# Optimization experiments

Hardware: AMD Instinct MI355X
Metric: run time of the kernel (lower is better)

## Reference

```python
import jax, jax.numpy as jnp
import numpy as np

EMBED = 768
HEADS = 12
HEAD_DIM = EMBED // HEADS
HIDDEN = int(EMBED * 4.0)
B, N = 2, 2048


def setup_inputs() -> dict:
    key = jax.random.key(0)
    ks = jax.random.split(key, 8)
    s = 0.02
    return {
        "x": jax.random.normal(ks[0], (B, N, EMBED), dtype=jnp.float32),
        "ln1_g": jnp.ones((EMBED,), jnp.float32),
        "ln1_b": jnp.zeros((EMBED,), jnp.float32),
        "qkv_w": jax.random.normal(ks[1], (3 * EMBED, EMBED), jnp.float32) * s,
        "qkv_b": jnp.zeros((3 * EMBED,), jnp.float32),
        "proj_w": jax.random.normal(ks[2], (EMBED, EMBED), jnp.float32) * s,
        "proj_b": jnp.zeros((EMBED,), jnp.float32),
        "ln2_g": jnp.ones((EMBED,), jnp.float32),
        "ln2_b": jnp.zeros((EMBED,), jnp.float32),
        "fc1_w": jax.random.normal(ks[3], (HIDDEN, EMBED), jnp.float32) * s,
        "fc1_b": jnp.zeros((HIDDEN,), jnp.float32),
        "fc2_w": jax.random.normal(ks[4], (EMBED, HIDDEN), jnp.float32) * s,
        "fc2_b": jnp.zeros((EMBED,), jnp.float32),
    }


def _layernorm(x, g, b, eps=1e-5):
    mu = jnp.mean(x, axis=-1, keepdims=True)
    var = jnp.var(x, axis=-1, keepdims=True)
    return (x - mu) * jax.lax.rsqrt(var + eps) * g + b


def reference(x, ln1_g, ln1_b, qkv_w, qkv_b, proj_w, proj_b,
              ln2_g, ln2_b, fc1_w, fc1_b, fc2_w, fc2_b):
    Bs, Ns, C = x.shape
    # --- attention (pre-norm) ---
    h = _layernorm(x, ln1_g, ln1_b)
    qkv = h @ qkv_w.T + qkv_b                      # [B,N,3C]
    qkv = qkv.reshape(Bs, Ns, 3, HEADS, HEAD_DIM)
    q, k, v = qkv[:, :, 0], qkv[:, :, 1], qkv[:, :, 2]   # [B,N,H,D]
    scale = HEAD_DIM ** -0.5
    attn = jnp.einsum('bqhd,bkhd->bhqk', q, k) * scale   # [B,H,N,N]
    attn = jax.nn.softmax(attn, axis=-1)
    o = jnp.einsum('bhqk,bkhd->bqhd', attn, v).reshape(Bs, Ns, C)
    x = x + (o @ proj_w.T + proj_b)
    # --- MLP (pre-norm) ---
    h = _layernorm(x, ln2_g, ln2_b)
    h = jax.nn.gelu(h @ fc1_w.T + fc1_b, approximate=False)  # torch GELU = erf
    x = x + (h @ fc2_w.T + fc2_b)
    return x
```

## Files before the change

kernel.cpp:

```cpp
#include <hip/hip_runtime.h>
#include <stdint.h>

#define EMBED  768
#define HEADS  12
#define HDIM   64
#define HIDDEN 3072
#define BSZ    2
#define SEQ    2048
#define NTOK   4096
#define QKVN   2304

typedef short short8 __attribute__((ext_vector_type(8)));
typedef float f32x4 __attribute__((ext_vector_type(4)));
typedef float float4v __attribute__((ext_vector_type(4)));
typedef unsigned short ushort4v __attribute__((ext_vector_type(4)));

__device__ __forceinline__ unsigned short f2bf(float f) {
    uint32_t x = __builtin_bit_cast(uint32_t, f);
    x = x + 0x7fffu + ((x >> 16) & 1u);
    return (unsigned short)(x >> 16);
}
__device__ __forceinline__ float bf2f(unsigned short u) {
    uint32_t x = ((uint32_t)u) << 16;
    return __builtin_bit_cast(float, x);
}
__device__ __forceinline__ void load16(const void* g, void* l) {
    __builtin_amdgcn_global_load_lds((const __attribute__((address_space(1))) void*)g,
                                     (__attribute__((address_space(3))) void*)l, 16, 0, 0);
}

__global__ __launch_bounds__(256) void cvt_k(const float* __restrict__ in,
                                             unsigned short* __restrict__ out, int n4) {
    int i = blockIdx.x * blockDim.x + threadIdx.x;
    int stride = gridDim.x * blockDim.x;
    for (; i < n4; i += stride) {
        float4v v = ((const float4v*)in)[i];
        ushort4v o;
#pragma unroll
        for (int j = 0; j < 4; j++) o[j] = f2bf(v[j]);
        ((ushort4v*)out)[i] = o;
    }
}

__global__ __launch_bounds__(256) void ln_k(const float* __restrict__ x,
                                            const float* __restrict__ g,
                                            const float* __restrict__ b,
                                            unsigned short* __restrict__ out) {
    const int row = blockIdx.x;
    const int t = threadIdx.x;
    const float* xr = x + (size_t)row * EMBED;
    float v0 = xr[t], v1 = xr[t + 256], v2 = xr[t + 512];
    float s = v0 + v1 + v2;
    float s2 = v0 * v0 + v1 * v1 + v2 * v2;
#pragma unroll
    for (int m = 1; m < 64; m <<= 1) { s += __shfl_xor(s, m); s2 += __shfl_xor(s2, m); }
    __shared__ float red[8];
    const int w = t >> 6;
    if ((t & 63) == 0) { red[w] = s; red[4 + w] = s2; }
    __syncthreads();
    s = red[0] + red[1] + red[2] + red[3];
    s2 = red[4] + red[5] + red[6] + red[7];
    const float mu = s * (1.0f / EMBED);
    const float var = s2 * (1.0f / EMBED) - mu * mu;
    const float rs = rsqrtf(var + 1e-5f);
    unsigned short* orow = out + (size_t)row * EMBED;
    orow[t]       = f2bf((v0 - mu) * rs * g[t]       + b[t]);
    orow[t + 256] = f2bf((v1 - mu) * rs * g[t + 256] + b[t + 256]);
    orow[t + 512] = f2bf((v2 - mu) * rs * g[t + 512] + b[t + 512]);
}

template <int EPI>
__global__ __launch_bounds__(256) void gemm_bt(const unsigned short* __restrict__ A,
                                               const unsigned short* __restrict__ W,
                                               const float* __restrict__ bias,
                                               const float* __restrict__ res,
                                               void* __restrict__ outp,
                                               unsigned short* __restrict__ vt,
                                               int M, int N, int K) {
    __shared__ __align__(16) unsigned short As[128 * 32];
    __shared__ __align__(16) unsigned short Bs[128 * 32];
    const int tid = threadIdx.x;
    const int w = tid >> 6, l = tid & 63;
    const int lr = l >> 4, lc = l & 15;
    const int nb = N >> 7;
    const int bx = blockIdx.x % nb, by = blockIdx.x / nb;
    const int row0 = by << 7, col0 = bx << 7;
    const int wr = w >> 1, wc = w & 1;
    const int srow = tid >> 2, skoff = (tid & 3) * 8;

    f32x4 acc[4][4] = {};

    const unsigned short* Ag0 = A + (size_t)(row0 + srow) * K + skoff;
    const unsigned short* Ag1 = A + (size_t)(row0 + 64 + srow) * K + skoff;
    const unsigned short* Wg0 = W + (size_t)(col0 + srow) * K + skoff;
    const unsigned short* Wg1 = W + (size_t)(col0 + 64 + srow) * K + skoff;
    unsigned short* la0 = &As[(size_t)tid * 8];
    unsigned short* la1 = la0 + 2048;
    unsigned short* lb0 = &Bs[(size_t)tid * 8];
    unsigned short* lb1 = lb0 + 2048;

    for (int k0 = 0; k0 < K; k0 += 32) {
        __syncthreads();
        load16(Ag0 + k0, la0);
        load16(Ag1 + k0, la1);
        load16(Wg0 + k0, lb0);
        load16(Wg1 + k0, lb1);
        __syncthreads();
        short8 af[4], bfr[4];
#pragma unroll
        for (int i = 0; i < 4; i++) af[i] = *(const short8*)&As[(wr * 64 + i * 16 + lc) * 32 + 8 * lr];
#pragma unroll
        for (int j = 0; j < 4; j++) bfr[j] = *(const short8*)&Bs[(wc * 64 + j * 16 + lc) * 32 + 8 * lr];
#pragma unroll
        for (int i = 0; i < 4; i++)
#pragma unroll
            for (int j = 0; j < 4; j++)
                acc[i][j] = __builtin_amdgcn_mfma_f32_16x16x32_bf16(af[i], bfr[j], acc[i][j], 0, 0, 0);
    }

#pragma unroll
    for (int i = 0; i < 4; i++) {
        const int r0 = row0 + wr * 64 + i * 16 + 4 * lr;
#pragma unroll
        for (int j = 0; j < 4; j++) {
            const int col = col0 + wc * 64 + j * 16 + lc;
            const float bv = bias[col];
            if (EPI == 0) {
                unsigned short* qo = (unsigned short*)outp;
                float v[4];
#pragma unroll
                for (int r = 0; r < 4; r++) {
                    v[r] = acc[i][j][r] + bv;
                    qo[(size_t)(r0 + r) * N + col] = f2bf(v[r]);
                }
                if (col >= 2 * EMBED) {
                    const int hh = (col - 2 * EMBED) >> 6, d = col & 63;
                    const int bb = r0 >> 11, n0 = r0 & (SEQ - 1);
                    ushort4v pk;
#pragma unroll
                    for (int r = 0; r < 4; r++) pk[r] = f2bf(v[r]);
                    *(ushort4v*)&vt[((size_t)(bb * HEADS + hh) * HDIM + d) * SEQ + n0] = pk;
                }
            } else if (EPI == 1 || EPI == 3) {
                float* fo = (float*)outp;
#pragma unroll
                for (int r = 0; r < 4; r++)
                    fo[(size_t)(r0 + r) * N + col] =
                        acc[i][j][r] + bv + res[(size_t)(r0 + r) * N + col];
            } else {
                unsigned short* qo = (unsigned short*)outp;
#pragma unroll
                for (int r = 0; r < 4; r++) {
                    float v = acc[i][j][r] + bv;
                    v = 0.5f * v * (1.0f + erff(v * 0.70710678118f));
                    qo[(size_t)(r0 + r) * N + col] = f2bf(v);
                }
            }
        }
    }
}

__global__ __launch_bounds__(256) void attn_k(const unsigned short* __restrict__ qkv,
                                              const unsigned short* __restrict__ vt,
                                              unsigned short* __restrict__ o_out) {
    __shared__ __align__(16) unsigned short Ks[128 * 64];
    __shared__ __align__(16) unsigned short Vs[64 * 128];
    __shared__ __align__(16) unsigned short Ps[4][16 * 136];

    const int tid = threadIdx.x;
    const int w = tid >> 6, l = tid & 63;
    const int lr = l >> 4, lc = l & 15;
    const int q0 = blockIdx.x * 64;
    const int bh = blockIdx.y;
    const int b = bh / HEADS, h = bh % HEADS;

    short8 aq[2];
#pragma unroll
    for (int kk = 0; kk < 2; kk++) {
        const int tok = b * SEQ + q0 + w * 16 + lc;
        aq[kk] = *(const short8*)&qkv[(size_t)tok * QKVN + h * HDIM + kk * 32 + 8 * lr];
    }

    f32x4 oacc[4] = {};
    float mst[4], lst[4];
#pragma unroll
    for (int r = 0; r < 4; r++) { mst[r] = -1e30f; lst[r] = 0.0f; }

    for (int kv0 = 0; kv0 < SEQ; kv0 += 128) {
        __syncthreads();
#pragma unroll
        for (int c = 0; c < 4; c++) {
            const int o = c * 4096 + tid * 16;
            const int krow = o >> 7, pc = o & 127;
            const int lcb = pc ^ ((krow & 7) << 4);
            load16(&qkv[(size_t)(b * SEQ + kv0 + krow) * QKVN + EMBED + h * HDIM + (lcb >> 1)],
                   (char*)Ks + o);
        }
#pragma unroll
        for (int c = 0; c < 4; c++) {
            const int o = c * 4096 + tid * 16;
            const int drow = o >> 8, pc = o & 255;
            const int lcb = pc ^ ((drow & 7) << 4);
            load16(&vt[(size_t)(bh * HDIM + drow) * SEQ + kv0 + (lcb >> 1)], (char*)Vs + o);
        }
        __syncthreads();

        f32x4 s[8] = {};
#pragma unroll
        for (int kk = 0; kk < 2; kk++) {
            short8 bk[8];
#pragma unroll
            for (int nj = 0; nj < 8; nj++) {
                const int krow = nj * 16 + lc;
                const int kb = kk * 64 + lr * 16;
                bk[nj] = *(const short8*)((const char*)Ks + krow * 128 + (kb ^ ((krow & 7) << 4)));
            }
#pragma unroll
            for (int nj = 0; nj < 8; nj++)
                s[nj] = __builtin_amdgcn_mfma_f32_16x16x32_bf16(aq[kk], bk[nj], s[nj], 0, 0, 0);
        }

#pragma unroll
        for (int r = 0; r < 4; r++) {
            float mt = s[0][r];
#pragma unroll
            for (int nj = 1; nj < 8; nj++) mt = fmaxf(mt, s[nj][r]);
#pragma unroll
            for (int m = 1; m < 16; m <<= 1) mt = fmaxf(mt, __shfl_xor(mt, m));
            const float mn = fmaxf(mst[r], mt);
            const float c_ = __expf((mst[r] - mn) * 0.125f);
            mst[r] = mn;
            float rsum = 0.0f;
#pragma unroll
            for (int nj = 0; nj < 8; nj++) {
                const float pv = __expf((s[nj][r] - mn) * 0.125f);
                s[nj][r] = pv;
                rsum += pv;
            }
#pragma unroll
            for (int m = 1; m < 16; m <<= 1) rsum += __shfl_xor(rsum, m);
            lst[r] = lst[r] * c_ + rsum;
#pragma unroll
            for (int dj = 0; dj < 4; dj++) oacc[dj][r] *= c_;
        }

#pragma unroll
        for (int nj = 0; nj < 8; nj++)
#pragma unroll
            for (int r = 0; r < 4; r++)
                Ps[w][(4 * lr + r) * 136 + nj * 16 + lc] = f2bf(s[nj][r]);

#pragma unroll
        for (int kk = 0; kk < 4; kk++) {
            short8 pa, bv[4];
            pa = *(const short8*)&Ps[w][lc * 136 + kk * 32 + 8 * lr];
#pragma unroll
            for (int dj = 0; dj < 4; dj++) {
                const int drow = dj * 16 + lc;
                const int kb = kk * 64 + lr * 16;
                bv[dj] = *(const short8*)((const char*)Vs + drow * 256 + (kb ^ ((drow & 7) << 4)));
            }
#pragma unroll
            for (int dj = 0; dj < 4; dj++)
                oacc[dj] = __builtin_amdgcn_mfma_f32_16x16x32_bf16(pa, bv[dj], oacc[dj], 0, 0, 0);
        }
    }

#pragma unroll
    for (int dj = 0; dj < 4; dj++)
#pragma unroll
        for (int r = 0; r < 4; r++) {
            const int q = q0 + w * 16 + 4 * lr + r;
            const int col = h * HDIM + dj * 16 + lc;
            o_out[(size_t)(b * SEQ + q) * EMBED + col] = f2bf(oacc[dj][r] / lst[r]);
        }
}

extern "C" void kernel_launch(void* const* d_in, const int* in_sizes, int n_in,
                              void* d_out, int out_size, void* d_ws, size_t ws_size,
                              hipStream_t stream) {
    const float* x      = (const float*)d_in[0];
    const float* ln1_g  = (const float*)d_in[1];
    const float* ln1_b  = (const float*)d_in[2];
    const float* qkv_w  = (const float*)d_in[3];
    const float* qkv_b  = (const float*)d_in[4];
    const float* proj_w = (const float*)d_in[5];
    const float* proj_b = (const float*)d_in[6];
    const float* ln2_g  = (const float*)d_in[7];
    const float* ln2_b  = (const float*)d_in[8];
    const float* fc1_w  = (const float*)d_in[9];
    const float* fc1_b  = (const float*)d_in[10];
    const float* fc2_w  = (const float*)d_in[11];
    const float* fc2_b  = (const float*)d_in[12];

    char* ws = (char*)d_ws;
    unsigned short* hbuf = (unsigned short*)(ws + 0);
    unsigned short* qkv  = (unsigned short*)(ws + 6291456);
    unsigned short* vt   = (unsigned short*)(ws + 25165824);
    float*          x2   = (float*)(ws + 31457280);
    unsigned short* gbuf = (unsigned short*)(ws + 6291456);
    unsigned short* wq   = (unsigned short*)(ws + 44040192);
    unsigned short* wp   = (unsigned short*)(ws + 47579136);
    unsigned short* w1   = (unsigned short*)(ws + 48758784);
    unsigned short* w2   = (unsigned short*)(ws + 53477376);

    {
        int n4;
        n4 = QKVN * EMBED / 4;
        cvt_k<<<dim3((n4 + 255) / 256 > 2048 ? 2048 : (n4 + 255) / 256), 256, 0, stream>>>(qkv_w, wq, n4);
        n4 = EMBED * EMBED / 4;
        cvt_k<<<dim3((n4 + 255) / 256 > 2048 ? 2048 : (n4 + 255) / 256), 256, 0, stream>>>(proj_w, wp, n4);
        n4 = HIDDEN * EMBED / 4;
        cvt_k<<<dim3((n4 + 255) / 256 > 2048 ? 2048 : (n4 + 255) / 256), 256, 0, stream>>>(fc1_w, w1, n4);
        n4 = EMBED * HIDDEN / 4;
        cvt_k<<<dim3((n4 + 255) / 256 > 2048 ? 2048 : (n4 + 255) / 256), 256, 0, stream>>>(fc2_w, w2, n4);
    }

    ln_k<<<dim3(NTOK), 256, 0, stream>>>(x, ln1_g, ln1_b, hbuf);

    gemm_bt<0><<<dim3((NTOK / 128) * (QKVN / 128)), 256, 0, stream>>>(
        hbuf, wq, qkv_b, nullptr, qkv, vt, NTOK, QKVN, EMBED);

    attn_k<<<dim3(SEQ / 64, BSZ * HEADS), 256, 0, stream>>>(qkv, vt, hbuf);

    gemm_bt<1><<<dim3((NTOK / 128) * (EMBED / 128)), 256, 0, stream>>>(
        hbuf, wp, proj_b, x, x2, nullptr, NTOK, EMBED, EMBED);

    ln_k<<<dim3(NTOK), 256, 0, stream>>>(x2, ln2_g, ln2_b, hbuf);

    gemm_bt<2><<<dim3((NTOK / 128) * (HIDDEN / 128)), 256, 0, stream>>>(
        hbuf, w1, fc1_b, nullptr, gbuf, nullptr, NTOK, HIDDEN, EMBED);

    gemm_bt<3><<<dim3((NTOK / 128) * (EMBED / 128)), 256, 0, stream>>>(
        gbuf, w2, fc2_b, x2, d_out, nullptr, NTOK, EMBED, HIDDEN);
}
```

Before: 356.0 us.

## Double-buffer GEMM LDS tiles, swizzle attention P buffer, merge weight conversions

The GEMM main loop now uses two LDS buffers and issues the next K-slice's global-to-LDS loads before computing on the current one, halving barriers per K step and overlapping loads with MFMA. The attention kernel's P scratch uses an XOR-swizzled byte layout to reduce LDS bank conflicts and converts fp32 to bf16 by truncation instead of round-to-nearest. The four weight-conversion launches are merged into one kernel. Risks: doubled LDS use may reduce occupancy, and truncated P rounding slightly changes numerics.

```diff
diff --git a/kernel.cpp b/kernel.cpp
--- a/kernel.cpp
+++ b/kernel.cpp
@@ -20,25 +20,29 @@
     x = x + 0x7fffu + ((x >> 16) & 1u);
     return (unsigned short)(x >> 16);
 }
-__device__ __forceinline__ float bf2f(unsigned short u) {
-    uint32_t x = ((uint32_t)u) << 16;
-    return __builtin_bit_cast(float, x);
-}
 __device__ __forceinline__ void load16(const void* g, void* l) {
     __builtin_amdgcn_global_load_lds((const __attribute__((address_space(1))) void*)g,
                                      (__attribute__((address_space(3))) void*)l, 16, 0, 0);
 }
 
-__global__ __launch_bounds__(256) void cvt_k(const float* __restrict__ in,
-                                             unsigned short* __restrict__ out, int n4) {
+__global__ __launch_bounds__(256) void cvt4_k(const float* __restrict__ s0, unsigned short* __restrict__ o0, int n0,
+                                              const float* __restrict__ s1, unsigned short* __restrict__ o1, int n1,
+                                              const float* __restrict__ s2, unsigned short* __restrict__ o2, int n2,
+                                              const float* __restrict__ s3, unsigned short* __restrict__ o3, int n3) {
     int i = blockIdx.x * blockDim.x + threadIdx.x;
-    int stride = gridDim.x * blockDim.x;
-    for (; i < n4; i += stride) {
-        float4v v = ((const float4v*)in)[i];
-        ushort4v o;
-#pragma unroll
-        for (int j = 0; j < 4; j++) o[j] = f2bf(v[j]);
-        ((ushort4v*)out)[i] = o;
+    const int stride = gridDim.x * blockDim.x;
+    const int tot = n0 + n1 + n2 + n3;
+    for (; i < tot; i += stride) {
+        const float* s; unsigned short* o; int j = i;
+        if (j < n0) { s = s0; o = o0; }
+        else if ((j -= n0) < n1) { s = s1; o = o1; }
+        else if ((j -= n1) < n2) { s = s2; o = o2; }
+        else { j -= n2; s = s3; o = o3; }
+        float4v v = ((const float4v*)s)[j];
+        ushort4v u;
+#pragma unroll
+        for (int t = 0; t < 4; t++) u[t] = f2bf(v[t]);
+        ((ushort4v*)o)[j] = u;
     }
 }
 
@@ -77,8 +81,8 @@
                                                void* __restrict__ outp,
                                                unsigned short* __restrict__ vt,
                                                int M, int N, int K) {
-    __shared__ __align__(16) unsigned short As[128 * 32];
-    __shared__ __align__(16) unsigned short Bs[128 * 32];
+    __shared__ __align__(16) unsigned short As[2][128 * 32];
+    __shared__ __align__(16) unsigned short Bs[2][128 * 32];
     const int tid = threadIdx.x;
     const int w = tid >> 6, l = tid & 63;
     const int lr = l >> 4, lc = l & 15;
@@ -94,28 +98,34 @@
     const unsigned short* Ag1 = A + (size_t)(row0 + 64 + srow) * K + skoff;
     const unsigned short* Wg0 = W + (size_t)(col0 + srow) * K + skoff;
     const unsigned short* Wg1 = W + (size_t)(col0 + 64 + srow) * K + skoff;
-    unsigned short* la0 = &As[(size_t)tid * 8];
-    unsigned short* la1 = la0 + 2048;
-    unsigned short* lb0 = &Bs[(size_t)tid * 8];
-    unsigned short* lb1 = lb0 + 2048;
-
-    for (int k0 = 0; k0 < K; k0 += 32) {
-        __syncthreads();
-        load16(Ag0 + k0, la0);
-        load16(Ag1 + k0, la1);
-        load16(Wg0 + k0, lb0);
-        load16(Wg1 + k0, lb1);
-        __syncthreads();
+
+    auto stage = [&](int buf, int k0) {
+        load16(Ag0 + k0, &As[buf][tid * 8]);
+        load16(Ag1 + k0, &As[buf][2048 + tid * 8]);
+        load16(Wg0 + k0, &Bs[buf][tid * 8]);
+        load16(Wg1 + k0, &Bs[buf][2048 + tid * 8]);
+    };
+    auto compute = [&](int buf) {
         short8 af[4], bfr[4];
 #pragma unroll
-        for (int i = 0; i < 4; i++) af[i] = *(const short8*)&As[(wr * 64 + i * 16 + lc) * 32 + 8 * lr];
-#pragma unroll
-        for (int j = 0; j < 4; j++) bfr[j] = *(const short8*)&Bs[(wc * 64 + j * 16 + lc) * 32 + 8 * lr];
+        for (int i = 0; i < 4; i++) af[i] = *(const short8*)&As[buf][(wr * 64 + i * 16 + lc) * 32 + 8 * lr];
+#pragma unroll
+        for (int j = 0; j < 4; j++) bfr[j] = *(const short8*)&Bs[buf][(wc * 64 + j * 16 + lc) * 32 + 8 * lr];
 #pragma unroll
         for (int i = 0; i < 4; i++)
 #pragma unroll
             for (int j = 0; j < 4; j++)
                 acc[i][j] = __builtin_amdgcn_mfma_f32_16x16x32_bf16(af[i], bfr[j], acc[i][j], 0, 0, 0);
+    };
+
+    stage(0, 0);
+    for (int k0 = 0; k0 < K; k0 += 64) {
+        __syncthreads();
+        stage(1, k0 + 32);
+        compute(0);
+        __syncthreads();
+        if (k0 + 64 < K) stage(0, k0 + 64);
+        compute(1);
     }
 
 #pragma unroll
@@ -165,7 +175,7 @@
                                               unsigned short* __restrict__ o_out) {
     __shared__ __align__(16) unsigned short Ks[128 * 64];
     __shared__ __align__(16) unsigned short Vs[64 * 128];
-    __shared__ __align__(16) unsigned short Ps[4][16 * 136];
+    __shared__ __align__(16) char Ps[4 * 16 * 272];
 
     const int tid = threadIdx.x;
     const int w = tid >> 6, l = tid & 63;
@@ -173,6 +183,7 @@
     const int q0 = blockIdx.x * 64;
     const int bh = blockIdx.y;
     const int b = bh / HEADS, h = bh % HEADS;
+    char* Pw = Ps + w * 4352;
 
     short8 aq[2];
 #pragma unroll
@@ -247,13 +258,17 @@
 #pragma unroll
         for (int nj = 0; nj < 8; nj++)
 #pragma unroll
-            for (int r = 0; r < 4; r++)
-                Ps[w][(4 * lr + r) * 136 + nj * 16 + lc] = f2bf(s[nj][r]);
+            for (int r = 0; r < 4; r++) {
+                const int q = 4 * lr + r;
+                const int kvb = (nj * 16 + lc) * 2;
+                *(unsigned short*)(Pw + q * 272 + (kvb ^ (q << 4))) =
+                    (unsigned short)(__builtin_bit_cast(uint32_t, s[nj][r]) >> 16);
+            }
 
 #pragma unroll
         for (int kk = 0; kk < 4; kk++) {
             short8 pa, bv[4];
-            pa = *(const short8*)&Ps[w][lc * 136 + kk * 32 + 8 * lr];
+            pa = *(const short8*)(Pw + lc * 272 + ((kk * 64 + 16 * lr) ^ (lc << 4)));
 #pragma unroll
             for (int dj = 0; dj < 4; dj++) {
                 const int drow = dj * 16 + lc;
@@ -304,17 +319,10 @@
     unsigned short* w1   = (unsigned short*)(ws + 48758784);
     unsigned short* w2   = (unsigned short*)(ws + 53477376);
 
-    {
-        int n4;
-        n4 = QKVN * EMBED / 4;
-        cvt_k<<<dim3((n4 + 255) / 256 > 2048 ? 2048 : (n4 + 255) / 256), 256, 0, stream>>>(qkv_w, wq, n4);
-        n4 = EMBED * EMBED / 4;
-        cvt_k<<<dim3((n4 + 255) / 256 > 2048 ? 2048 : (n4 + 255) / 256), 256, 0, stream>>>(proj_w, wp, n4);
-        n4 = HIDDEN * EMBED / 4;
-        cvt_k<<<dim3((n4 + 255) / 256 > 2048 ? 2048 : (n4 + 255) / 256), 256, 0, stream>>>(fc1_w, w1, n4);
-        n4 = EMBED * HIDDEN / 4;
-        cvt_k<<<dim3((n4 + 255) / 256 > 2048 ? 2048 : (n4 + 255) / 256), 256, 0, stream>>>(fc2_w, w2, n4);
-    }
+    cvt4_k<<<dim3(2048), 256, 0, stream>>>(qkv_w, wq, QKVN * EMBED / 4,
+                                           proj_w, wp, EMBED * EMBED / 4,
+                                           fc1_w, w1, HIDDEN * EMBED / 4,
+                                           fc2_w, w2, EMBED * HIDDEN / 4);
 
     ln_k<<<dim3(NTOK), 256, 0, stream>>>(x, ln1_g, ln1_b, hbuf);
 
```

Result: slower. 394.6 us (+10.9%).
